# Kernel tuning notes

Measured on AMD Instinct MI355X. Metric: run time of the kernel, lower is better.

Reference implementation:

```python
import jax, jax.numpy as jnp
import numpy as np

HIDDEN = 128
HEADS = 8
HEAD_DIM = HIDDEN // HEADS
N_BLOCKS = 2048
N_EDGES = 4096


def setup_inputs() -> dict:
    key = jax.random.key(0)
    ks = jax.random.split(key, 14)
    s = 0.02
    return {
        "block_features": jax.random.normal(ks[0], (N_BLOCKS, HIDDEN), dtype=jnp.float32),
        "edge_indices": jax.random.randint(ks[1], (2, N_EDGES), 0, N_BLOCKS, dtype=jnp.int32),
        # edge_encoder: Linear(2H->H), ReLU, Linear(H->H)
        "W_e1": jax.random.normal(ks[2], (2 * HIDDEN, HIDDEN), dtype=jnp.float32) * s,
        "b_e1": jnp.zeros((HIDDEN,), dtype=jnp.float32),
        "W_e2": jax.random.normal(ks[3], (HIDDEN, HIDDEN), dtype=jnp.float32) * s,
        "b_e2": jnp.zeros((HIDDEN,), dtype=jnp.float32),
        "Wq": jax.random.normal(ks[4], (HIDDEN, HIDDEN), dtype=jnp.float32) * s,
        "bq": jnp.zeros((HIDDEN,), dtype=jnp.float32),
        "Wk": jax.random.normal(ks[5], (HIDDEN, HIDDEN), dtype=jnp.float32) * s,
        "bk": jnp.zeros((HIDDEN,), dtype=jnp.float32),
        "Wv": jax.random.normal(ks[6], (HIDDEN, HIDDEN), dtype=jnp.float32) * s,
        "bv": jnp.zeros((HIDDEN,), dtype=jnp.float32),
        "Wo": jax.random.normal(ks[7], (HIDDEN, HIDDEN), dtype=jnp.float32) * s,
        "bo": jnp.zeros((HIDDEN,), dtype=jnp.float32),
    }


def reference(block_features, edge_indices, W_e1, b_e1, W_e2, b_e2,
              Wq, bq, Wk, bk, Wv, bv, Wo, bo):
    n_blocks = block_features.shape[0]
    src_idx, dst_idx = edge_indices[0], edge_indices[1]

    # gather src/dst node features, concat -> edge MLP (dropout is identity in eval)
    ef = jnp.concatenate([block_features[src_idx], block_features[dst_idx]], axis=1)  # [E, 2H]
    ef = jnp.maximum(ef @ W_e1 + b_e1, 0.0) @ W_e2 + b_e2  # [E, H]

    E = ef.shape[0]
    scale = HEAD_DIM ** -0.5
    q = (ef @ Wq + bq).reshape(E, HEADS, HEAD_DIM)
    k = (ef @ Wk + bk).reshape(E, HEADS, HEAD_DIM)
    v = (ef @ Wv + bv).reshape(E, HEADS, HEAD_DIM)

    # dense attention over all edges
    scores = jnp.einsum("ehd,fhd->hef", q, k) * scale  # [H, E, E]
    attn = jax.nn.softmax(scores, axis=-1)
    attn_out = jnp.einsum("hef,fhd->ehd", attn, v).reshape(E, HIDDEN)
    updated_edges = attn_out @ Wo + bo  # [E, H]

    # scatter_sum back to destination nodes
    block_updates = jax.ops.segment_sum(updated_edges, dst_idx, num_segments=n_blocks)
    return block_features + block_updates
```

## Files before the change

### kernel.cpp

```cpp
#include <hip/hip_runtime.h>
#include <hip/hip_bf16.h>

#define NB 2048
#define NE 4096
#define HID 128
#define NHEAD 8
#define HD 16

#define QSCALE 0.36067376022224085f

typedef short s16x8 __attribute__((ext_vector_type(8)));
typedef float f32x4  __attribute__((ext_vector_type(4)));
typedef float f32x16 __attribute__((ext_vector_type(16)));

static __device__ __forceinline__ ushort f2bf(float x) {
    uint u = __builtin_bit_cast(uint, x);
    uint r = (u + 0x7fffu + ((u >> 16) & 1u)) >> 16;
    return (ushort)r;
}
static __device__ __forceinline__ uint pack2bf(float a, float b) {
    return (uint)f2bf(a) | ((uint)f2bf(b) << 16);
}
static __device__ __forceinline__ uint packrd(float a, float b) {
    uint ua = __builtin_bit_cast(uint, a) + 0x8000u;
    uint ub = __builtin_bit_cast(uint, b) + 0x8000u;
    return __builtin_amdgcn_perm(ub, ua, 0x07060302u);
}

__global__ __launch_bounds__(256) void convert_kernel(
    const float* __restrict__ We1, const float* __restrict__ We2,
    const float* __restrict__ Wq,  const float* __restrict__ Wk,
    const float* __restrict__ Wv,  const float* __restrict__ Wo,
    ushort* __restrict__ wb)
{
    int i = blockIdx.x * 256 + threadIdx.x;
    if (i < 8192) {
        int k = i >> 5, n4 = (i & 31) * 4;
        float4 t = *(const float4*)(We1 + k * HID + n4);
        wb[(n4 + 0) * 256 + k] = f2bf(t.x);
        wb[(n4 + 1) * 256 + k] = f2bf(t.y);
        wb[(n4 + 2) * 256 + k] = f2bf(t.z);
        wb[(n4 + 3) * 256 + k] = f2bf(t.w);
    } else if (i < 28672) {
        int j = i - 8192;
        int m = j >> 12;
        int r = j & 4095;
        int k = r >> 5, n4 = (r & 31) * 4;
        const float* W = (m == 0) ? We2 : (m == 1) ? Wq : (m == 2) ? Wk
                       : (m == 3) ? Wv : Wo;
        float4 t = *(const float4*)(W + k * HID + n4);
        ushort* o = wb + 32768 + m * 16384;
        o[(n4 + 0) * 128 + k] = f2bf(t.x);
        o[(n4 + 1) * 128 + k] = f2bf(t.y);
        o[(n4 + 2) * 128 + k] = f2bf(t.z);
        o[(n4 + 3) * 128 + k] = f2bf(t.w);
    }
}

__global__ __launch_bounds__(512, 2) void mlp_qkv_kernel(
    const float* __restrict__ bf, const int* __restrict__ src, const int* __restrict__ dst,
    const ushort* __restrict__ wb,
    const float* __restrict__ be1, const float* __restrict__ be2,
    const float* __restrict__ bq,  const float* __restrict__ bk, const float* __restrict__ bv,
    ushort* __restrict__ qg, ushort* __restrict__ kg, ushort* __restrict__ vT,
    float4* __restrict__ out_init)
{
    __shared__ ushort sX[16][264];
    __shared__ ushort sH[16][136];
    __shared__ ushort sE[16][136];

    const int tid = threadIdx.x;
    const int w   = tid >> 6;
    const int l   = tid & 63;
    const int lo16 = l & 15;
    const int hi4  = l >> 4;
    const int e0 = blockIdx.x * 16;

    if (tid < 256)
        out_init[blockIdx.x * 256 + tid] = ((const float4*)bf)[blockIdx.x * 256 + tid];

    const ushort* We1T = wb;
    const ushort* We2T = wb + 32768;
    const ushort* WqT  = wb + 49152;
    const ushort* WkT  = wb + 65536;
    const ushort* WvT  = wb + 81920;

    s16x8 B1[8], B2[4], BQ[4], BK[4], BV[4];
    #pragma unroll
    for (int k0 = 0; k0 < 8; k0++)
        B1[k0] = *(const s16x8*)(We1T + (w * 16 + lo16) * 256 + k0 * 32 + hi4 * 8);
    #pragma unroll
    for (int k0 = 0; k0 < 4; k0++) {
        B2[k0] = *(const s16x8*)(We2T + (w * 16 + lo16) * 128 + k0 * 32 + hi4 * 8);
        BQ[k0] = *(const s16x8*)(WqT  + (w * 16 + lo16) * 128 + k0 * 32 + hi4 * 8);
        BK[k0] = *(const s16x8*)(WkT  + (w * 16 + lo16) * 128 + k0 * 32 + hi4 * 8);
        BV[k0] = *(const s16x8*)(WvT  + (w * 16 + lo16) * 128 + k0 * 32 + hi4 * 8);
    }
    const float bias1 = be1[w * 16 + lo16];
    const float bias2 = be2[w * 16 + lo16];
    const float biasq = bq[w * 16 + lo16];
    const float biask = bk[w * 16 + lo16];
    const float biasv = bv[w * 16 + lo16];

    {
        const int r  = tid >> 5;
        const int sg = tid & 31;
        const int e  = e0 + r;
        const int node = (sg < 16) ? src[e] : dst[e];
        const float4* rowp = (const float4*)(bf + node * HID);
        const int fb = (sg & 15) * 2;
        float4 t0 = rowp[fb], t1 = rowp[fb + 1];
        *(uint2*)&sX[r][sg * 8]     = make_uint2(pack2bf(t0.x, t0.y), pack2bf(t0.z, t0.w));
        *(uint2*)&sX[r][sg * 8 + 4] = make_uint2(pack2bf(t1.x, t1.y), pack2bf(t1.z, t1.w));
    }
    __syncthreads();

    f32x4 acc;

    {
        acc = (f32x4){bias1, bias1, bias1, bias1};
        #pragma unroll
        for (int k0 = 0; k0 < 8; k0++) {
            s16x8 a = *(const s16x8*)&sX[lo16][k0 * 32 + hi4 * 8];
            acc = __builtin_amdgcn_mfma_f32_16x16x32_bf16(a, B1[k0], acc, 0, 0, 0);
        }
        #pragma unroll
        for (int r = 0; r < 4; r++)
            sH[hi4 * 4 + r][w * 16 + lo16] = f2bf(fmaxf(acc[r], 0.0f));
    }
    __syncthreads();

    {
        acc = (f32x4){bias2, bias2, bias2, bias2};
        #pragma unroll
        for (int k0 = 0; k0 < 4; k0++) {
            s16x8 a = *(const s16x8*)&sH[lo16][k0 * 32 + hi4 * 8];
            acc = __builtin_amdgcn_mfma_f32_16x16x32_bf16(a, B2[k0], acc, 0, 0, 0);
        }
        #pragma unroll
        for (int r = 0; r < 4; r++)
            sE[hi4 * 4 + r][w * 16 + lo16] = f2bf(acc[r]);
    }
    __syncthreads();

#define PROJ(BARR, BIAS, STORE) do { \
    acc = (f32x4){BIAS, BIAS, BIAS, BIAS}; \
    _Pragma("unroll") \
    for (int k0 = 0; k0 < 4; k0++) { \
        s16x8 a = *(const s16x8*)&sE[lo16][k0 * 32 + hi4 * 8]; \
        acc = __builtin_amdgcn_mfma_f32_16x16x32_bf16(a, BARR[k0], acc, 0, 0, 0); \
    } \
    _Pragma("unroll") \
    for (int r = 0; r < 4; r++) { STORE; } \
} while (0)

    PROJ(BQ, biasq, { int e = e0 + hi4 * 4 + r;
                      qg[(w * NE + e) * 16 + lo16] = f2bf(acc[r] * QSCALE); });
    PROJ(BK, biask, { int e = e0 + hi4 * 4 + r;
                      kg[(w * NE + e) * 16 + lo16] = f2bf(acc[r]); });
    PROJ(BV, biasv, { int e = e0 + hi4 * 4 + r;
                      vT[(w * 16 + lo16) * NE + e] = f2bf(acc[r]); });
#undef PROJ
}

__global__ __launch_bounds__(512, 8) void attn_kernel(
    const ushort* __restrict__ qg, const ushort* __restrict__ kg,
    const ushort* __restrict__ vT, ushort* __restrict__ Og)
{
    __shared__ ushort Pbuf[8][2048];

    const int tid = threadIdx.x;
    const int w   = tid >> 6;
    const int l   = tid & 63;
    const int h   = blockIdx.y;
    const int q0  = blockIdx.x * 32;
    const int lo16 = l & 15, hi4 = l >> 4;
    const int lo32 = l & 31, hi2 = l >> 5;

    ushort* Pw = &Pbuf[w][0];

    const s16x8 qf = *(const s16x8*)(qg + (h * NE + q0 + lo32) * 16 + hi2 * 8);

    const f32x16 z16 = {};
    f32x4 o0 = {0,0,0,0}, o1 = {0,0,0,0};
    float L = 0.0f;

    const int kbase = w * (NE / 8);
    const ushort* kp = kg + (size_t)h * NE * 16;
    const ushort* vp = vT + (size_t)(h * 16 + lo16) * NE;

    #pragma unroll 2
    for (int kt = 0; kt < 16; kt++) {
        const int key0 = kbase + kt * 32;
        s16x8 kc = *(const s16x8*)(kp + (key0 + lo32) * 16 + hi2 * 8);
        s16x8 vc = *(const s16x8*)(vp + key0 + hi4 * 8);

        f32x16 s = __builtin_amdgcn_mfma_f32_32x32x16_bf16(kc, qf, z16, 0, 0, 0);

        float e[16];
        #pragma unroll
        for (int i = 0; i < 16; i++) { e[i] = __builtin_amdgcn_exp2f(s[i]); L += e[i]; }

        const int b8 = (kt & 1) * 8;
        #pragma unroll
        for (int g = 0; g < 4; g++) {
            uint2 w2 = make_uint2(packrd(e[4*g], e[4*g+1]), packrd(e[4*g+2], e[4*g+3]));
            *(uint2*)&Pw[((b8 + 2*g + hi2) * 32 + lo32) * 4] = w2;
        }

        uint2 alo = *(const uint2*)&Pw[((b8 + 2*hi4)     * 32 + lo16) * 4];
        uint2 ahi = *(const uint2*)&Pw[((b8 + 2*hi4 + 1) * 32 + lo16) * 4];
        uint2 blo = *(const uint2*)&Pw[((b8 + 2*hi4)     * 32 + 16 + lo16) * 4];
        uint2 bhi = *(const uint2*)&Pw[((b8 + 2*hi4 + 1) * 32 + 16 + lo16) * 4];
        s16x8 pb0 = __builtin_bit_cast(s16x8, make_uint4(alo.x, alo.y, ahi.x, ahi.y));
        s16x8 pb1 = __builtin_bit_cast(s16x8, make_uint4(blo.x, blo.y, bhi.x, bhi.y));

        o0 = __builtin_amdgcn_mfma_f32_16x16x32_bf16(vc, pb0, o0, 0, 0, 0);
        o1 = __builtin_amdgcn_mfma_f32_16x16x32_bf16(vc, pb1, o1, 0, 0, 0);
    }

    float Lf = L + __shfl_xor(L, 32, 64);

    __syncthreads();
    float* sO = (float*)&Pbuf[0][0];
    #pragma unroll
    for (int r = 0; r < 4; r++) {
        sO[(w * 32 + lo16) * 18 + hi4 * 4 + r]      = o0[r];
        sO[(w * 32 + 16 + lo16) * 18 + hi4 * 4 + r] = o1[r];
    }
    if (hi2 == 0) sO[(w * 32 + lo32) * 18 + 16] = Lf;
    __syncthreads();

    {
        const int q = tid >> 4;
        const int d = tid & 15;
        float sum = 0.0f, Lq = 0.0f;
        #pragma unroll
        for (int ww = 0; ww < 8; ww++) {
            sum += sO[(ww * 32 + q) * 18 + d];
            Lq  += sO[(ww * 32 + q) * 18 + 16];
        }
        Og[(q0 + q) * HID + h * 16 + d] = f2bf(sum / Lq);
    }
}

__global__ __launch_bounds__(512, 2) void wo_scatter_kernel(
    const ushort* __restrict__ Og, const ushort* __restrict__ wb,
    const float* __restrict__ bo, const int* __restrict__ dst,
    float* __restrict__ out)
{
    const int tid = threadIdx.x;
    const int w   = tid >> 6;
    const int l   = tid & 63;
    const int lo16 = l & 15, hi4 = l >> 4;
    const int e0 = blockIdx.x * 16;
    const ushort* WoT = wb + 98304;

    s16x8 BO[4], AO[4];
    #pragma unroll
    for (int k0 = 0; k0 < 4; k0++) {
        BO[k0] = *(const s16x8*)(WoT + (w * 16 + lo16) * 128 + k0 * 32 + hi4 * 8);
        AO[k0] = *(const s16x8*)(Og + (e0 + lo16) * HID + k0 * 32 + hi4 * 8);
    }
    int dste[4];
    #pragma unroll
    for (int r = 0; r < 4; r++) dste[r] = dst[e0 + hi4 * 4 + r];
    const float b_ = bo[w * 16 + lo16];

    f32x4 acc = (f32x4){b_, b_, b_, b_};
    #pragma unroll
    for (int k0 = 0; k0 < 4; k0++)
        acc = __builtin_amdgcn_mfma_f32_16x16x32_bf16(AO[k0], BO[k0], acc, 0, 0, 0);

    #pragma unroll
    for (int r = 0; r < 4; r++) {
        atomicAdd(out + dste[r] * HID + w * 16 + lo16, acc[r]);
    }
}

extern "C" void kernel_launch(void* const* d_in, const int* in_sizes, int n_in,
                              void* d_out, int out_size, void* d_ws, size_t ws_size,
                              hipStream_t stream)
{
    const float* bf  = (const float*)d_in[0];
    const int*   ei  = (const int*)d_in[1];
    const int*   src = ei;
    const int*   dst = ei + NE;
    const float* We1 = (const float*)d_in[2];
    const float* be1 = (const float*)d_in[3];
    const float* We2 = (const float*)d_in[4];
    const float* be2 = (const float*)d_in[5];
    const float* Wq  = (const float*)d_in[6];
    const float* bq  = (const float*)d_in[7];
    const float* Wk  = (const float*)d_in[8];
    const float* bk  = (const float*)d_in[9];
    const float* Wv  = (const float*)d_in[10];
    const float* bv  = (const float*)d_in[11];
    const float* Wo  = (const float*)d_in[12];
    const float* bo  = (const float*)d_in[13];

    char* ws = (char*)d_ws;
    ushort* wb  = (ushort*)(ws);
    ushort* qg  = (ushort*)(ws + (1u<<18));
    ushort* kg  = (ushort*)(ws + (1u<<18) + (1u<<20));
    ushort* vT  = (ushort*)(ws + (1u<<18) + (2u<<20));
    ushort* Og  = (ushort*)(ws + (1u<<18) + (3u<<20));

    convert_kernel<<<112, 256, 0, stream>>>(We1, We2, Wq, Wk, Wv, Wo, wb);
    mlp_qkv_kernel<<<NE / 16, 512, 0, stream>>>(bf, src, dst, wb, be1, be2, bq, bk, bv,
                                                qg, kg, vT, (float4*)d_out);
    attn_kernel<<<dim3(NE / 32, NHEAD), 512, 0, stream>>>(qg, kg, vT, Og);
    wo_scatter_kernel<<<NE / 16, 512, 0, stream>>>(Og, wb, bo, dst, (float*)d_out);
}
```

Before: 47.89 us.

## Process 64 queries per attention block to reuse K/V tile loads

The attention kernel now handles two 32-query groups per block, so each K and V fragment loaded from global memory feeds two score MFMAs and four PV MFMAs instead of one and two. This halves the grid and the total K/V traffic per head. In exchange the per-wave shared P buffer doubles, register pressure rises, and the launch-bounds occupancy hint of 8 is dropped, which may lower occupancy and latency hiding. The grid also shrinks to 512 blocks, which lowers parallelism across CUs.

Measured after the change: 48.91 us. +2.1%, slower.

```diff
diff --git a/kernel.cpp b/kernel.cpp
--- a/kernel.cpp
+++ b/kernel.cpp
@@ -163,27 +163,28 @@
 #undef PROJ
 }
 
-__global__ __launch_bounds__(512, 8) void attn_kernel(
+__global__ __launch_bounds__(512) void attn_kernel(
     const ushort* __restrict__ qg, const ushort* __restrict__ kg,
     const ushort* __restrict__ vT, ushort* __restrict__ Og)
 {
-    __shared__ ushort Pbuf[8][2048];
+    __shared__ ushort Pbuf[8][4096];
 
     const int tid = threadIdx.x;
     const int w   = tid >> 6;
     const int l   = tid & 63;
     const int h   = blockIdx.y;
-    const int q0  = blockIdx.x * 32;
+    const int q0  = blockIdx.x * 64;
     const int lo16 = l & 15, hi4 = l >> 4;
     const int lo32 = l & 31, hi2 = l >> 5;
 
     ushort* Pw = &Pbuf[w][0];
 
-    const s16x8 qf = *(const s16x8*)(qg + (h * NE + q0 + lo32) * 16 + hi2 * 8);
+    const s16x8 qfA = *(const s16x8*)(qg + (h * NE + q0 + lo32) * 16 + hi2 * 8);
+    const s16x8 qfB = *(const s16x8*)(qg + (h * NE + q0 + 32 + lo32) * 16 + hi2 * 8);
 
     const f32x16 z16 = {};
-    f32x4 o0 = {0,0,0,0}, o1 = {0,0,0,0};
-    float L = 0.0f;
+    f32x4 o0 = {0,0,0,0}, o1 = {0,0,0,0}, o2 = {0,0,0,0}, o3 = {0,0,0,0};
+    float LA = 0.0f, LB = 0.0f;
 
     const int kbase = w * (NE / 8);
     const ushort* kp = kg + (size_t)h * NE * 16;
@@ -194,53 +195,75 @@
         const int key0 = kbase + kt * 32;
         s16x8 kc = *(const s16x8*)(kp + (key0 + lo32) * 16 + hi2 * 8);
         s16x8 vc = *(const s16x8*)(vp + key0 + hi4 * 8);
-
-        f32x16 s = __builtin_amdgcn_mfma_f32_32x32x16_bf16(kc, qf, z16, 0, 0, 0);
-
-        float e[16];
-        #pragma unroll
-        for (int i = 0; i < 16; i++) { e[i] = __builtin_amdgcn_exp2f(s[i]); L += e[i]; }
-
         const int b8 = (kt & 1) * 8;
-        #pragma unroll
-        for (int g = 0; g < 4; g++) {
-            uint2 w2 = make_uint2(packrd(e[4*g], e[4*g+1]), packrd(e[4*g+2], e[4*g+3]));
-            *(uint2*)&Pw[((b8 + 2*g + hi2) * 32 + lo32) * 4] = w2;
-        }
-
-        uint2 alo = *(const uint2*)&Pw[((b8 + 2*hi4)     * 32 + lo16) * 4];
-        uint2 ahi = *(const uint2*)&Pw[((b8 + 2*hi4 + 1) * 32 + lo16) * 4];
-        uint2 blo = *(const uint2*)&Pw[((b8 + 2*hi4)     * 32 + 16 + lo16) * 4];
-        uint2 bhi = *(const uint2*)&Pw[((b8 + 2*hi4 + 1) * 32 + 16 + lo16) * 4];
-        s16x8 pb0 = __builtin_bit_cast(s16x8, make_uint4(alo.x, alo.y, ahi.x, ahi.y));
-        s16x8 pb1 = __builtin_bit_cast(s16x8, make_uint4(blo.x, blo.y, bhi.x, bhi.y));
-
-        o0 = __builtin_amdgcn_mfma_f32_16x16x32_bf16(vc, pb0, o0, 0, 0, 0);
-        o1 = __builtin_amdgcn_mfma_f32_16x16x32_bf16(vc, pb1, o1, 0, 0, 0);
-    }
-
-    float Lf = L + __shfl_xor(L, 32, 64);
+
+        {
+            f32x16 s = __builtin_amdgcn_mfma_f32_32x32x16_bf16(kc, qfA, z16, 0, 0, 0);
+            float e[16];
+            #pragma unroll
+            for (int i = 0; i < 16; i++) { e[i] = __builtin_amdgcn_exp2f(s[i]); LA += e[i]; }
+            #pragma unroll
+            for (int g = 0; g < 4; g++) {
+                uint2 w2 = make_uint2(packrd(e[4*g], e[4*g+1]), packrd(e[4*g+2], e[4*g+3]));
+                *(uint2*)&Pw[((b8 + 2*g + hi2) * 64 + lo32) * 4] = w2;
+            }
+        }
+        {
+            f32x16 s = __builtin_amdgcn_mfma_f32_32x32x16_bf16(kc, qfB, z16, 0, 0, 0);
+            float e[16];
+            #pragma unroll
+            for (int i = 0; i < 16; i++) { e[i] = __builtin_amdgcn_exp2f(s[i]); LB += e[i]; }
+            #pragma unroll
+            for (int g = 0; g < 4; g++) {
+                uint2 w2 = make_uint2(packrd(e[4*g], e[4*g+1]), packrd(e[4*g+2], e[4*g+3]));
+                *(uint2*)&Pw[((b8 + 2*g + hi2) * 64 + 32 + lo32) * 4] = w2;
+            }
+        }
+
+        #define PVQ(oX, qc) do { \
+            uint2 plo = *(const uint2*)&Pw[((b8 + 2*hi4)     * 64 + (qc)) * 4]; \
+            uint2 phi = *(const uint2*)&Pw[((b8 + 2*hi4 + 1) * 64 + (qc)) * 4]; \
+            s16x8 pb = __builtin_bit_cast(s16x8, make_uint4(plo.x, plo.y, phi.x, phi.y)); \
+            oX = __builtin_amdgcn_mfma_f32_16x16x32_bf16(vc, pb, oX, 0, 0, 0); \
+        } while (0)
+        PVQ(o0, lo16);
+        PVQ(o1, 16 + lo16);
+        PVQ(o2, 32 + lo16);
+        PVQ(o3, 48 + lo16);
+        #undef PVQ
+    }
+
+    float LfA = LA + __shfl_xor(LA, 32, 64);
+    float LfB = LB + __shfl_xor(LB, 32, 64);
 
     __syncthreads();
     float* sO = (float*)&Pbuf[0][0];
     #pragma unroll
     for (int r = 0; r < 4; r++) {
-        sO[(w * 32 + lo16) * 18 + hi4 * 4 + r]      = o0[r];
-        sO[(w * 32 + 16 + lo16) * 18 + hi4 * 4 + r] = o1[r];
-    }
-    if (hi2 == 0) sO[(w * 32 + lo32) * 18 + 16] = Lf;
+        sO[(w * 64 + lo16) * 18 + hi4 * 4 + r]      = o0[r];
+        sO[(w * 64 + 16 + lo16) * 18 + hi4 * 4 + r] = o1[r];
+        sO[(w * 64 + 32 + lo16) * 18 + hi4 * 4 + r] = o2[r];
+        sO[(w * 64 + 48 + lo16) * 18 + hi4 * 4 + r] = o3[r];
+    }
+    if (hi2 == 0) {
+        sO[(w * 64 + lo32) * 18 + 16]      = LfA;
+        sO[(w * 64 + 32 + lo32) * 18 + 16] = LfB;
+    }
     __syncthreads();
 
     {
-        const int q = tid >> 4;
         const int d = tid & 15;
-        float sum = 0.0f, Lq = 0.0f;
-        #pragma unroll
-        for (int ww = 0; ww < 8; ww++) {
-            sum += sO[(ww * 32 + q) * 18 + d];
-            Lq  += sO[(ww * 32 + q) * 18 + 16];
-        }
-        Og[(q0 + q) * HID + h * 16 + d] = f2bf(sum / Lq);
+        #pragma unroll
+        for (int half = 0; half < 2; half++) {
+            const int q = (tid >> 4) + half * 32;
+            float sum = 0.0f, Lq = 0.0f;
+            #pragma unroll
+            for (int ww = 0; ww < 8; ww++) {
+                sum += sO[(ww * 64 + q) * 18 + d];
+                Lq  += sO[(ww * 64 + q) * 18 + 16];
+            }
+            Og[(q0 + q) * HID + h * 16 + d] = f2bf(sum / Lq);
+        }
     }
 }
 
@@ -309,6 +332,6 @@
     convert_kernel<<<112, 256, 0, stream>>>(We1, We2, Wq, Wk, Wv, Wo, wb);
     mlp_qkv_kernel<<<NE / 16, 512, 0, stream>>>(bf, src, dst, wb, be1, be2, bq, bk, bv,
                                                 qg, kg, vT, (float4*)d_out);
-    attn_kernel<<<dim3(NE / 32, NHEAD), 512, 0, stream>>>(qg, kg, vT, Og);
+    attn_kernel<<<dim3(NE / 64, NHEAD), 512, 0, stream>>>(qg, kg, vT, Og);
     wo_scatter_kernel<<<NE / 16, 512, 0, stream>>>(Og, wb, bo, dst, (float*)d_out);
 }
```
